# Kernel optimization log

Measured on AMD Instinct MI355X. Metric: run time of the kernel, lower is better.

Reference implementation:

```python
import jax, jax.numpy as jnp
import numpy as np


def setup_inputs() -> dict:
    key = jax.random.key(0)
    k1, k2 = jax.random.split(key)
    B, DIM, T, SIZE = 64, 512, 2048, 1024
    H = jax.random.normal(k1, (B, DIM, T), dtype=jnp.float32)
    units = jax.random.normal(k2, (DIM, SIZE), dtype=jnp.float32)
    return {"H": H, "units": units}


def reference(H, units):
    # H: (B, dim, T), units: (dim, size)
    # Original: C[b, s, t] = exp(-||H[b,:,t] - units[:,s]||^2) normalized over s.
    # exp(-d^2) / sum_s exp(-d^2) == softmax(-d^2, axis=s).
    Ht = jnp.swapaxes(H, 1, 2)                      # (B, T, dim)
    h_sq = jnp.sum(Ht * Ht, axis=-1, keepdims=True)  # (B, T, 1)
    m_sq = jnp.sum(units * units, axis=0)            # (size,)
    cross = jnp.einsum('btd,ds->bts', Ht, units)     # (B, T, size) GEMM
    sqdist = h_sq - 2.0 * cross + m_sq               # (B, T, size)
    C = jax.nn.softmax(-sqdist, axis=-1)             # normalize over codebook
    return jnp.swapaxes(C, 1, 2)                     # (B, size, T)
```

## Files before the change

### kernel.cpp

```cpp
#include <hip/hip_runtime.h>
#include <stdint.h>


typedef unsigned short u16;
typedef __attribute__((ext_vector_type(8))) short short8;
typedef __attribute__((ext_vector_type(4))) float f32x4;

#define B_DIM 64
#define DIM   512
#define T_DIM 2048
#define S_DIM 1024

#define SLOT   40960
#define A_LO   16384
#define B_HI   32768
#define B_LO   36864
#define MSQ_O  122880
#define REDM_O 126976
#define REDS_O 128000
#define SM_SZ  129024

__device__ __forceinline__ u16 f32_to_bf16(float f) {
  uint32_t u = __float_as_uint(f);
  uint32_t r = u + 0x7FFFu + ((u >> 16) & 1u);
  return (u16)(r >> 16);
}
__device__ __forceinline__ float bf16_to_f32(u16 h) {
  return __uint_as_float(((uint32_t)h) << 16);
}

__global__ __launch_bounds__(256) void k_prep_units(const float* __restrict__ units,
                                                    u16* __restrict__ Uh, u16* __restrict__ Ul,
                                                    float* __restrict__ msq) {
  const int s0 = blockIdx.x * 4;
  const int tid = threadIdx.x;
  const int lane = tid & 63, wv = tid >> 6;
  float acc0 = 0.f, acc1 = 0.f, acc2 = 0.f, acc3 = 0.f;
#pragma unroll
  for (int j = 0; j < 2; ++j) {
    const int d = tid + j * 256;
    const float4 v = *(const float4*)(units + (size_t)d * S_DIM + s0);
    acc0 += v.x * v.x; acc1 += v.y * v.y; acc2 += v.z * v.z; acc3 += v.w * v.w;
    u16 h;
    h = f32_to_bf16(v.x); Uh[(s0 + 0) * DIM + d] = h; Ul[(s0 + 0) * DIM + d] = f32_to_bf16(v.x - bf16_to_f32(h));
    h = f32_to_bf16(v.y); Uh[(s0 + 1) * DIM + d] = h; Ul[(s0 + 1) * DIM + d] = f32_to_bf16(v.y - bf16_to_f32(h));
    h = f32_to_bf16(v.z); Uh[(s0 + 2) * DIM + d] = h; Ul[(s0 + 2) * DIM + d] = f32_to_bf16(v.z - bf16_to_f32(h));
    h = f32_to_bf16(v.w); Uh[(s0 + 3) * DIM + d] = h; Ul[(s0 + 3) * DIM + d] = f32_to_bf16(v.w - bf16_to_f32(h));
  }
#pragma unroll
  for (int off = 1; off < 64; off <<= 1) {
    acc0 += __shfl_xor(acc0, off);
    acc1 += __shfl_xor(acc1, off);
    acc2 += __shfl_xor(acc2, off);
    acc3 += __shfl_xor(acc3, off);
  }
  __shared__ float part[4][4];
  if (lane == 0) { part[wv][0] = acc0; part[wv][1] = acc1; part[wv][2] = acc2; part[wv][3] = acc3; }
  __syncthreads();
  if (tid < 4) msq[s0 + tid] = part[0][tid] + part[1][tid] + part[2][tid] + part[3][tid];
}

__global__ __launch_bounds__(256) void k_prep_h(const float* __restrict__ H,
                                                u16* __restrict__ Hh, u16* __restrict__ Hl) {
  __shared__ float tile[64 * 68];
  const int t0 = blockIdx.x * 64, d0 = blockIdx.y * 64, b = blockIdx.z;
  const int tid = threadIdx.x;
#pragma unroll
  for (int j = 0; j < 4; ++j) {
    const int chunk = tid + j * 256;
    const int r = chunk >> 4, c4 = (chunk & 15) * 4;
    const float4 v = *(const float4*)(H + ((size_t)(b * DIM + d0 + r)) * T_DIM + t0 + c4);
    *(float4*)(&tile[r * 68 + c4]) = v;
  }
  __syncthreads();
#pragma unroll
  for (int j = 0; j < 2; ++j) {
    const int chunk = tid + j * 256;
    const int q = chunk >> 3, e8 = (chunk & 7) * 8;
    union { u16 us[8]; uint4 v4; } hi, lo;
#pragma unroll
    for (int k = 0; k < 8; ++k) {
      const float f = tile[(e8 + k) * 68 + q];
      const u16 h = f32_to_bf16(f);
      hi.us[k] = h;
      lo.us[k] = f32_to_bf16(f - bf16_to_f32(h));
    }
    const size_t o = ((size_t)(b * T_DIM + t0 + q)) * DIM + d0 + e8;
    *(uint4*)(Hh + o) = hi.v4;
    *(uint4*)(Hl + o) = lo.v4;
  }
}

__device__ __forceinline__ void gl16(const void* g, void* l) {
  __builtin_amdgcn_global_load_lds((const __attribute__((address_space(1))) void*)g,
                                   (__attribute__((address_space(3))) void*)l, 16, 0, 0);
}

#define WAITV(N) asm volatile("s_waitcnt vmcnt(" #N ")" ::: "memory")
#define SYNCPT() do { __builtin_amdgcn_s_barrier(); __builtin_amdgcn_sched_barrier(0); } while (0)
#define LGKM0()  do { asm volatile("s_waitcnt lgkmcnt(0)" ::: "memory"); __builtin_amdgcn_sched_barrier(0); } while (0)

__global__ __launch_bounds__(512, 2) void k_fused(const u16* __restrict__ Uh, const u16* __restrict__ Ul,
                                                  const u16* __restrict__ Hh, const u16* __restrict__ Hl,
                                                  const float* __restrict__ msq,
                                                  float* __restrict__ out) {
  __shared__ __align__(16) char sm[SM_SZ];
  const int tid = threadIdx.x;
  const int lane = tid & 63, wv = tid >> 6;
  const int sw = wv >> 1, tw = wv & 1;
  const int l15 = lane & 15, lhi = lane >> 4;

  const int t00 = blockIdx.x * 64;
  const int bb = blockIdx.y;

  const int rA0 = tid >> 2;
  const int csA = ((tid & 3) ^ (rA0 >> 1)) & 3;
  const size_t aBase0 = (size_t)rA0 * 1024 + (size_t)csA * 16;
  const size_t aBase1 = aBase0 + (size_t)128 * 1024;
  const int rB = (tid & 255) >> 2;
  const int csB = ((tid & 3) ^ (rB >> 1)) & 3;
  const size_t bBase = ((size_t)(bb * T_DIM + t00 + rB)) * 1024 + (size_t)csB * 16;
  const char* const pAh = (const char*)Uh;
  const char* const pAl = (const char*)Ul;
  const char* const pB  = (tid < 256) ? (const char*)Hh : (const char*)Hl;
  const int dT = tid * 16;

#define STAGE(SLOTBASE, J2) do {                                          \
    const size_t aoff = (size_t)((J2) >> 4) * 262144 + (size_t)((J2) & 15) * 64; \
    const size_t boff = (size_t)((J2) & 15) * 64;                         \
    char* d = (SLOTBASE);                                                 \
    gl16(pAh + aBase0 + aoff, d + dT);                                    \
    gl16(pAh + aBase1 + aoff, d + dT + 8192);                             \
    gl16(pAl + aBase0 + aoff, d + A_LO + dT);                             \
    gl16(pAl + aBase1 + aoff, d + A_LO + dT + 8192);                      \
    gl16(pB + bBase + boff, d + B_HI + dT);                               \
  } while (0)

  const int cidx = ((lhi) ^ (l15 >> 1)) & 3;
  const int offA = sw * 4096 + l15 * 64 + cidx * 16;
  const int offB = tw * 2048 + l15 * 64 + cidx * 16;

  f32x4 acc[4][4][2];
#pragma unroll
  for (int sc = 0; sc < 4; ++sc)
#pragma unroll
    for (int mt = 0; mt < 4; ++mt)
#pragma unroll
      for (int nt = 0; nt < 2; ++nt)
        acc[sc][mt][nt] = (f32x4){0.f, 0.f, 0.f, 0.f};

#define COMPUTE(SC) do {                                                  \
    const char* sl = sm + slotJ * SLOT;                                   \
    short8 ah[4], al[4], bh[2], bl[2];                                    \
    _Pragma("unroll") for (int mt = 0; mt < 4; ++mt) {                    \
      ah[mt] = *(const short8*)(sl + offA + mt * 1024);                   \
      al[mt] = *(const short8*)(sl + A_LO + offA + mt * 1024);            \
    }                                                                     \
    _Pragma("unroll") for (int nt = 0; nt < 2; ++nt) {                    \
      bh[nt] = *(const short8*)(sl + B_HI + offB + nt * 1024);            \
      bl[nt] = *(const short8*)(sl + B_LO + offB + nt * 1024);            \
    }                                                                     \
    LGKM0();                                                              \
    __builtin_amdgcn_s_setprio(1);                                        \
    _Pragma("unroll") for (int mt = 0; mt < 4; ++mt)                      \
      _Pragma("unroll") for (int nt = 0; nt < 2; ++nt) {                  \
        acc[SC][mt][nt] = __builtin_amdgcn_mfma_f32_16x16x32_bf16(ah[mt], bh[nt], acc[SC][mt][nt], 0, 0, 0); \
        acc[SC][mt][nt] = __builtin_amdgcn_mfma_f32_16x16x32_bf16(ah[mt], bl[nt], acc[SC][mt][nt], 0, 0, 0); \
        acc[SC][mt][nt] = __builtin_amdgcn_mfma_f32_16x16x32_bf16(al[mt], bh[nt], acc[SC][mt][nt], 0, 0, 0); \
      }                                                                   \
    __builtin_amdgcn_s_setprio(0);                                        \
  } while (0)

  if (tid < 256) gl16((const char*)msq + tid * 16, sm + MSQ_O + tid * 16);
  STAGE(sm + 0 * SLOT, 0);
  STAGE(sm + 1 * SLOT, 1);

  int slotJ = 0;
#pragma unroll
  for (int sc = 0; sc < 3; ++sc) {
#pragma unroll 1
    for (int k = 0; k < 16; ++k) {
      const int j = sc * 16 + k;
      int slot2 = slotJ + 2; if (slot2 >= 3) slot2 -= 3;
      STAGE(sm + slot2 * SLOT, j + 2);
      WAITV(10); SYNCPT();
      COMPUTE(sc);
      SYNCPT();
      slotJ = (slotJ == 2) ? 0 : slotJ + 1;
    }
  }
#pragma unroll 1
  for (int k = 0; k < 14; ++k) {
    const int j = 48 + k;
    int slot2 = slotJ + 2; if (slot2 >= 3) slot2 -= 3;
    STAGE(sm + slot2 * SLOT, j + 2);
    WAITV(10); SYNCPT();
    COMPUTE(3);
    SYNCPT();
    slotJ = (slotJ == 2) ? 0 : slotJ + 1;
  }
  WAITV(5); SYNCPT(); COMPUTE(3); SYNCPT();
  slotJ = (slotJ == 2) ? 0 : slotJ + 1;
  WAITV(0); SYNCPT(); COMPUTE(3); SYNCPT();

  const float* msql = (const float*)(sm + MSQ_O);
  float* redM = (float*)(sm + REDM_O);
  float* redS = (float*)(sm + REDS_O);

  float m0 = -3.0e38f, m1 = -3.0e38f;
#pragma unroll
  for (int sc = 0; sc < 4; ++sc)
#pragma unroll
    for (int mt = 0; mt < 4; ++mt) {
      const int sb = sc * 256 + sw * 64 + mt * 16 + lhi * 4;
      const f32x4 q = *(const f32x4*)(msql + sb);
#pragma unroll
      for (int r = 0; r < 4; ++r) {
        const float v0 = 2.f * acc[sc][mt][0][r] - q[r];
        const float v1 = 2.f * acc[sc][mt][1][r] - q[r];
        acc[sc][mt][0][r] = v0; acc[sc][mt][1][r] = v1;
        m0 = fmaxf(m0, v0); m1 = fmaxf(m1, v1);
      }
    }
  m0 = fmaxf(m0, __shfl_xor(m0, 16)); m0 = fmaxf(m0, __shfl_xor(m0, 32));
  m1 = fmaxf(m1, __shfl_xor(m1, 16)); m1 = fmaxf(m1, __shfl_xor(m1, 32));
  if (lane < 16) { redM[wv * 32 + lane] = m0; redM[wv * 32 + 16 + lane] = m1; }
  __syncthreads();
  float M0 = redM[tw * 32 + l15], M1 = redM[tw * 32 + 16 + l15];
#pragma unroll
  for (int w = 1; w < 4; ++w) {
    M0 = fmaxf(M0, redM[(tw + 2 * w) * 32 + l15]);
    M1 = fmaxf(M1, redM[(tw + 2 * w) * 32 + 16 + l15]);
  }
  float s0 = 0.f, s1 = 0.f;
#pragma unroll
  for (int sc = 0; sc < 4; ++sc)
#pragma unroll
    for (int mt = 0; mt < 4; ++mt)
#pragma unroll
      for (int r = 0; r < 4; ++r) {
        const float e0 = __expf(acc[sc][mt][0][r] - M0);
        const float e1 = __expf(acc[sc][mt][1][r] - M1);
        acc[sc][mt][0][r] = e0; acc[sc][mt][1][r] = e1;
        s0 += e0; s1 += e1;
      }
  s0 += __shfl_xor(s0, 16); s0 += __shfl_xor(s0, 32);
  s1 += __shfl_xor(s1, 16); s1 += __shfl_xor(s1, 32);
  if (lane < 16) { redS[wv * 32 + lane] = s0; redS[wv * 32 + 16 + lane] = s1; }
  __syncthreads();
  float S0 = redS[tw * 32 + l15], S1 = redS[tw * 32 + 16 + l15];
#pragma unroll
  for (int w = 1; w < 4; ++w) {
    S0 += redS[(tw + 2 * w) * 32 + l15];
    S1 += redS[(tw + 2 * w) * 32 + 16 + l15];
  }
  const float r0 = 1.0f / S0, r1 = 1.0f / S1;

  float* const outb = out + ((size_t)bb << 21);
  const int tbase = t00 + tw * 32 + l15;
#pragma unroll
  for (int sc = 0; sc < 4; ++sc)
#pragma unroll
    for (int mt = 0; mt < 4; ++mt) {
      const int sb = sc * 256 + sw * 64 + mt * 16 + lhi * 4;
#pragma unroll
      for (int r = 0; r < 4; ++r) {
        outb[(size_t)(sb + r) * T_DIM + tbase]      = acc[sc][mt][0][r] * r0;
        outb[(size_t)(sb + r) * T_DIM + tbase + 16] = acc[sc][mt][1][r] * r1;
      }
    }
}

extern "C" void kernel_launch(void* const* d_in, const int* in_sizes, int n_in,
                              void* d_out, int out_size, void* d_ws, size_t ws_size,
                              hipStream_t stream) {
  (void)in_sizes; (void)n_in; (void)out_size; (void)ws_size;
  const float* H = (const float*)d_in[0];
  const float* units = (const float*)d_in[1];
  float* out = (float*)d_out;
  char* ws = (char*)d_ws;
  u16* Hh = (u16*)(ws);
  u16* Hl = (u16*)(ws + 134217728);
  u16* Uh = (u16*)(ws + 268435456);
  u16* Ul = (u16*)(ws + 269484032);
  float* msq = (float*)(ws + 270532608);

  k_prep_units<<<dim3(S_DIM / 4), 256, 0, stream>>>(units, Uh, Ul, msq);
  k_prep_h<<<dim3(T_DIM / 64, DIM / 64, B_DIM), 256, 0, stream>>>(H, Hh, Hl);
  k_fused<<<dim3(T_DIM / 64, B_DIM), 512, 0, stream>>>(Uh, Ul, Hh, Hl, msq, out);
}
```

Measured before the change: 680.1 us.

## Switch fused GEMM-softmax to 32x32x16 MFMA with full-S tiles and double buffering

Replaces the 16x16x32 MFMA tiling, which walked four S-chunks across a 3-slot pipeline, with 32x32x16 MFMAs. Each of the 8 waves now owns 128 codebook rows over all 64 t-columns, with a 2-slot double buffer over K steps of 16 and a new LDS layout. The goal is fewer MFMA instructions and LDS reads per FLOP, plus a simpler reduction over 8 waves. In exchange it drops the LDS swizzle and the explicit lgkmcnt wait, so bank conflicts are possible, and LDS use grows, which may hurt the 2-blocks-per-CU occupancy target.

```diff
diff --git a/kernel.cpp b/kernel.cpp
--- a/kernel.cpp
+++ b/kernel.cpp
@@ -5,20 +5,20 @@
 typedef unsigned short u16;
 typedef __attribute__((ext_vector_type(8))) short short8;
 typedef __attribute__((ext_vector_type(4))) float f32x4;
+typedef __attribute__((ext_vector_type(16))) float f32x16;
 
 #define B_DIM 64
 #define DIM   512
 #define T_DIM 2048
 #define S_DIM 1024
 
-#define SLOT   40960
-#define A_LO   16384
-#define B_HI   32768
-#define B_LO   36864
-#define MSQ_O  122880
-#define REDM_O 126976
-#define REDS_O 128000
-#define SM_SZ  129024
+#define SLOT   69632
+#define A_LO   32768
+#define B_HI   65536
+#define MSQ_O  139264
+#define REDM_O 143360
+#define REDS_O 145408
+#define SM_SZ  147456
 
 __device__ __forceinline__ u16 f32_to_bf16(float f) {
   uint32_t u = __float_as_uint(f);
@@ -98,7 +98,6 @@
 
 #define WAITV(N) asm volatile("s_waitcnt vmcnt(" #N ")" ::: "memory")
 #define SYNCPT() do { __builtin_amdgcn_s_barrier(); __builtin_amdgcn_sched_barrier(0); } while (0)
-#define LGKM0()  do { asm volatile("s_waitcnt lgkmcnt(0)" ::: "memory"); __builtin_amdgcn_sched_barrier(0); } while (0)
 
 __global__ __launch_bounds__(512, 2) void k_fused(const u16* __restrict__ Uh, const u16* __restrict__ Ul,
                                                   const u16* __restrict__ Hh, const u16* __restrict__ Hl,
@@ -107,168 +106,158 @@
   __shared__ __align__(16) char sm[SM_SZ];
   const int tid = threadIdx.x;
   const int lane = tid & 63, wv = tid >> 6;
-  const int sw = wv >> 1, tw = wv & 1;
-  const int l15 = lane & 15, lhi = lane >> 4;
+  const int l31 = lane & 31, lhi = lane >> 5;
+  const int lane16 = lane * 16;
 
   const int t00 = blockIdx.x * 64;
   const int bb = blockIdx.y;
 
-  const int rA0 = tid >> 2;
-  const int csA = ((tid & 3) ^ (rA0 >> 1)) & 3;
-  const size_t aBase0 = (size_t)rA0 * 1024 + (size_t)csA * 16;
-  const size_t aBase1 = aBase0 + (size_t)128 * 1024;
-  const int rB = (tid & 255) >> 2;
-  const int csB = ((tid & 3) ^ (rB >> 1)) & 3;
-  const size_t bBase = ((size_t)(bb * T_DIM + t00 + rB)) * 1024 + (size_t)csB * 16;
+  int aSrc[4], aDst[4];
+#pragma unroll
+  for (int i = 0; i < 4; ++i) {
+    const int ci = tid + i * 512;
+    const int si = (ci >> 6) * 32 + (ci & 31);
+    aSrc[i] = si * 1024 + (((ci >> 5) & 1) << 4);
+    aDst[i] = ci * 16;
+  }
+  const int cB = tid & 127;
+  const int tB = (cB >> 6) * 32 + (cB & 31);
+  const size_t bSrc = ((size_t)(bb * T_DIM + t00 + tB)) * 1024 + (size_t)(((cB >> 5) & 1) << 4);
+  const int bDst = B_HI + tid * 16;
   const char* const pAh = (const char*)Uh;
   const char* const pAl = (const char*)Ul;
-  const char* const pB  = (tid < 256) ? (const char*)Hh : (const char*)Hl;
-  const int dT = tid * 16;
-
-#define STAGE(SLOTBASE, J2) do {                                          \
-    const size_t aoff = (size_t)((J2) >> 4) * 262144 + (size_t)((J2) & 15) * 64; \
-    const size_t boff = (size_t)((J2) & 15) * 64;                         \
-    char* d = (SLOTBASE);                                                 \
-    gl16(pAh + aBase0 + aoff, d + dT);                                    \
-    gl16(pAh + aBase1 + aoff, d + dT + 8192);                             \
-    gl16(pAl + aBase0 + aoff, d + A_LO + dT);                             \
-    gl16(pAl + aBase1 + aoff, d + A_LO + dT + 8192);                      \
-    gl16(pB + bBase + boff, d + B_HI + dT);                               \
+  const char* const pBsel = (tid < 128) ? (const char*)Hh : (const char*)Hl;
+
+#define STAGE(SLOTB, KS) do {                                             \
+    const int ko = (KS) * 32;                                             \
+    char* d = sm + (SLOTB);                                               \
+    gl16(pAh + aSrc[0] + ko, d + aDst[0]);                                \
+    gl16(pAh + aSrc[1] + ko, d + aDst[1]);                                \
+    gl16(pAh + aSrc[2] + ko, d + aDst[2]);                                \
+    gl16(pAh + aSrc[3] + ko, d + aDst[3]);                                \
+    gl16(pAl + aSrc[0] + ko, d + A_LO + aDst[0]);                         \
+    gl16(pAl + aSrc[1] + ko, d + A_LO + aDst[1]);                         \
+    gl16(pAl + aSrc[2] + ko, d + A_LO + aDst[2]);                         \
+    gl16(pAl + aSrc[3] + ko, d + A_LO + aDst[3]);                         \
+    if (tid < 256) gl16(pBsel + bSrc + ko, d + bDst);                     \
   } while (0)
 
-  const int cidx = ((lhi) ^ (l15 >> 1)) & 3;
-  const int offA = sw * 4096 + l15 * 64 + cidx * 16;
-  const int offB = tw * 2048 + l15 * 64 + cidx * 16;
-
-  f32x4 acc[4][4][2];
-#pragma unroll
-  for (int sc = 0; sc < 4; ++sc)
-#pragma unroll
-    for (int mt = 0; mt < 4; ++mt)
-#pragma unroll
-      for (int nt = 0; nt < 2; ++nt)
-        acc[sc][mt][nt] = (f32x4){0.f, 0.f, 0.f, 0.f};
-
-#define COMPUTE(SC) do {                                                  \
-    const char* sl = sm + slotJ * SLOT;                                   \
+  const int sw = wv;
+
+  f32x16 acc[4][2];
+#pragma unroll
+  for (int mt = 0; mt < 4; ++mt)
+#pragma unroll
+    for (int nt = 0; nt < 2; ++nt)
+#pragma unroll
+      for (int r = 0; r < 16; ++r)
+        acc[mt][nt][r] = 0.f;
+
+#define COMPUTE(SLOTB) do {                                               \
+    const char* sl = sm + (SLOTB);                                        \
     short8 ah[4], al[4], bh[2], bl[2];                                    \
     _Pragma("unroll") for (int mt = 0; mt < 4; ++mt) {                    \
-      ah[mt] = *(const short8*)(sl + offA + mt * 1024);                   \
-      al[mt] = *(const short8*)(sl + A_LO + offA + mt * 1024);            \
+      ah[mt] = *(const short8*)(sl + (sw * 4 + mt) * 1024 + lane16);      \
+      al[mt] = *(const short8*)(sl + A_LO + (sw * 4 + mt) * 1024 + lane16); \
     }                                                                     \
     _Pragma("unroll") for (int nt = 0; nt < 2; ++nt) {                    \
-      bh[nt] = *(const short8*)(sl + B_HI + offB + nt * 1024);            \
-      bl[nt] = *(const short8*)(sl + B_LO + offB + nt * 1024);            \
+      bh[nt] = *(const short8*)(sl + B_HI + nt * 1024 + lane16);          \
+      bl[nt] = *(const short8*)(sl + B_HI + 2048 + nt * 1024 + lane16);   \
     }                                                                     \
-    LGKM0();                                                              \
     __builtin_amdgcn_s_setprio(1);                                        \
     _Pragma("unroll") for (int mt = 0; mt < 4; ++mt)                      \
       _Pragma("unroll") for (int nt = 0; nt < 2; ++nt) {                  \
-        acc[SC][mt][nt] = __builtin_amdgcn_mfma_f32_16x16x32_bf16(ah[mt], bh[nt], acc[SC][mt][nt], 0, 0, 0); \
-        acc[SC][mt][nt] = __builtin_amdgcn_mfma_f32_16x16x32_bf16(ah[mt], bl[nt], acc[SC][mt][nt], 0, 0, 0); \
-        acc[SC][mt][nt] = __builtin_amdgcn_mfma_f32_16x16x32_bf16(al[mt], bh[nt], acc[SC][mt][nt], 0, 0, 0); \
+        acc[mt][nt] = __builtin_amdgcn_mfma_f32_32x32x16_bf16(ah[mt], bh[nt], acc[mt][nt], 0, 0, 0); \
+        acc[mt][nt] = __builtin_amdgcn_mfma_f32_32x32x16_bf16(ah[mt], bl[nt], acc[mt][nt], 0, 0, 0); \
+        acc[mt][nt] = __builtin_amdgcn_mfma_f32_32x32x16_bf16(al[mt], bh[nt], acc[mt][nt], 0, 0, 0); \
       }                                                                   \
     __builtin_amdgcn_s_setprio(0);                                        \
   } while (0)
 
   if (tid < 256) gl16((const char*)msq + tid * 16, sm + MSQ_O + tid * 16);
-  STAGE(sm + 0 * SLOT, 0);
-  STAGE(sm + 1 * SLOT, 1);
-
-  int slotJ = 0;
-#pragma unroll
-  for (int sc = 0; sc < 3; ++sc) {
+  STAGE(0, 0);
+  STAGE(SLOT, 1);
+
 #pragma unroll 1
-    for (int k = 0; k < 16; ++k) {
-      const int j = sc * 16 + k;
-      int slot2 = slotJ + 2; if (slot2 >= 3) slot2 -= 3;
-      STAGE(sm + slot2 * SLOT, j + 2);
-      WAITV(10); SYNCPT();
-      COMPUTE(sc);
-      SYNCPT();
-      slotJ = (slotJ == 2) ? 0 : slotJ + 1;
-    }
-  }
-#pragma unroll 1
-  for (int k = 0; k < 14; ++k) {
-    const int j = 48 + k;
-    int slot2 = slotJ + 2; if (slot2 >= 3) slot2 -= 3;
-    STAGE(sm + slot2 * SLOT, j + 2);
-    WAITV(10); SYNCPT();
-    COMPUTE(3);
+  for (int k = 0; k < 31; ++k) {
+    WAITV(8);
     SYNCPT();
-    slotJ = (slotJ == 2) ? 0 : slotJ + 1;
-  }
-  WAITV(5); SYNCPT(); COMPUTE(3); SYNCPT();
-  slotJ = (slotJ == 2) ? 0 : slotJ + 1;
-  WAITV(0); SYNCPT(); COMPUTE(3); SYNCPT();
+    COMPUTE((k & 1) * SLOT);
+    SYNCPT();
+    if (k < 30) STAGE((k & 1) * SLOT, k + 2);
+  }
+  WAITV(0);
+  SYNCPT();
+  COMPUTE(SLOT);
 
   const float* msql = (const float*)(sm + MSQ_O);
   float* redM = (float*)(sm + REDM_O);
   float* redS = (float*)(sm + REDS_O);
 
-  float m0 = -3.0e38f, m1 = -3.0e38f;
-#pragma unroll
-  for (int sc = 0; sc < 4; ++sc)
-#pragma unroll
-    for (int mt = 0; mt < 4; ++mt) {
-      const int sb = sc * 256 + sw * 64 + mt * 16 + lhi * 4;
-      const f32x4 q = *(const f32x4*)(msql + sb);
+  float mx0 = -3.0e38f, mx1 = -3.0e38f;
+#pragma unroll
+  for (int mt = 0; mt < 4; ++mt) {
+    const int sb = sw * 128 + mt * 32 + lhi * 4;
+#pragma unroll
+    for (int q = 0; q < 4; ++q) {
+      const f32x4 mq = *(const f32x4*)(msql + sb + q * 8);
 #pragma unroll
       for (int r = 0; r < 4; ++r) {
-        const float v0 = 2.f * acc[sc][mt][0][r] - q[r];
-        const float v1 = 2.f * acc[sc][mt][1][r] - q[r];
-        acc[sc][mt][0][r] = v0; acc[sc][mt][1][r] = v1;
-        m0 = fmaxf(m0, v0); m1 = fmaxf(m1, v1);
+        const int reg = q * 4 + r;
+        const float v0 = 2.f * acc[mt][0][reg] - mq[r];
+        const float v1 = 2.f * acc[mt][1][reg] - mq[r];
+        acc[mt][0][reg] = v0; acc[mt][1][reg] = v1;
+        mx0 = fmaxf(mx0, v0); mx1 = fmaxf(mx1, v1);
       }
     }
-  m0 = fmaxf(m0, __shfl_xor(m0, 16)); m0 = fmaxf(m0, __shfl_xor(m0, 32));
-  m1 = fmaxf(m1, __shfl_xor(m1, 16)); m1 = fmaxf(m1, __shfl_xor(m1, 32));
-  if (lane < 16) { redM[wv * 32 + lane] = m0; redM[wv * 32 + 16 + lane] = m1; }
-  __syncthreads();
-  float M0 = redM[tw * 32 + l15], M1 = redM[tw * 32 + 16 + l15];
-#pragma unroll
-  for (int w = 1; w < 4; ++w) {
-    M0 = fmaxf(M0, redM[(tw + 2 * w) * 32 + l15]);
-    M1 = fmaxf(M1, redM[(tw + 2 * w) * 32 + 16 + l15]);
+  }
+  mx0 = fmaxf(mx0, __shfl_xor(mx0, 32));
+  mx1 = fmaxf(mx1, __shfl_xor(mx1, 32));
+  if (lane < 32) { redM[wv * 64 + l31] = mx0; redM[wv * 64 + 32 + l31] = mx1; }
+  __syncthreads();
+  float M0 = redM[l31], M1 = redM[32 + l31];
+#pragma unroll
+  for (int w = 1; w < 8; ++w) {
+    M0 = fmaxf(M0, redM[w * 64 + l31]);
+    M1 = fmaxf(M1, redM[w * 64 + 32 + l31]);
   }
   float s0 = 0.f, s1 = 0.f;
 #pragma unroll
-  for (int sc = 0; sc < 4; ++sc)
-#pragma unroll
-    for (int mt = 0; mt < 4; ++mt)
+  for (int mt = 0; mt < 4; ++mt)
+#pragma unroll
+    for (int reg = 0; reg < 16; ++reg) {
+      const float e0 = __expf(acc[mt][0][reg] - M0);
+      const float e1 = __expf(acc[mt][1][reg] - M1);
+      acc[mt][0][reg] = e0; acc[mt][1][reg] = e1;
+      s0 += e0; s1 += e1;
+    }
+  s0 += __shfl_xor(s0, 32);
+  s1 += __shfl_xor(s1, 32);
+  if (lane < 32) { redS[wv * 64 + l31] = s0; redS[wv * 64 + 32 + l31] = s1; }
+  __syncthreads();
+  float S0 = redS[l31], S1 = redS[32 + l31];
+#pragma unroll
+  for (int w = 1; w < 8; ++w) {
+    S0 += redS[w * 64 + l31];
+    S1 += redS[w * 64 + 32 + l31];
+  }
+  const float r0 = 1.0f / S0, r1 = 1.0f / S1;
+
+  float* const outb = out + ((size_t)bb << 21);
+  const int tc0 = t00 + l31, tc1 = t00 + 32 + l31;
+#pragma unroll
+  for (int mt = 0; mt < 4; ++mt) {
+    const int sb = sw * 128 + mt * 32 + lhi * 4;
+#pragma unroll
+    for (int q = 0; q < 4; ++q)
 #pragma unroll
       for (int r = 0; r < 4; ++r) {
-        const float e0 = __expf(acc[sc][mt][0][r] - M0);
-        const float e1 = __expf(acc[sc][mt][1][r] - M1);
-        acc[sc][mt][0][r] = e0; acc[sc][mt][1][r] = e1;
-        s0 += e0; s1 += e1;
+        const int srow = sb + q * 8 + r;
+        const int reg = q * 4 + r;
+        outb[(size_t)srow * T_DIM + tc0] = acc[mt][0][reg] * r0;
+        outb[(size_t)srow * T_DIM + tc1] = acc[mt][1][reg] * r1;
       }
-  s0 += __shfl_xor(s0, 16); s0 += __shfl_xor(s0, 32);
-  s1 += __shfl_xor(s1, 16); s1 += __shfl_xor(s1, 32);
-  if (lane < 16) { redS[wv * 32 + lane] = s0; redS[wv * 32 + 16 + lane] = s1; }
-  __syncthreads();
-  float S0 = redS[tw * 32 + l15], S1 = redS[tw * 32 + 16 + l15];
-#pragma unroll
-  for (int w = 1; w < 4; ++w) {
-    S0 += redS[(tw + 2 * w) * 32 + l15];
-    S1 += redS[(tw + 2 * w) * 32 + 16 + l15];
-  }
-  const float r0 = 1.0f / S0, r1 = 1.0f / S1;
-
-  float* const outb = out + ((size_t)bb << 21);
-  const int tbase = t00 + tw * 32 + l15;
-#pragma unroll
-  for (int sc = 0; sc < 4; ++sc)
-#pragma unroll
-    for (int mt = 0; mt < 4; ++mt) {
-      const int sb = sc * 256 + sw * 64 + mt * 16 + lhi * 4;
-#pragma unroll
-      for (int r = 0; r < 4; ++r) {
-        outb[(size_t)(sb + r) * T_DIM + tbase]      = acc[sc][mt][0][r] * r0;
-        outb[(size_t)(sb + r) * T_DIM + tbase + 16] = acc[sc][mt][1][r] * r1;
-      }
-    }
+  }
 }
 
 extern "C" void kernel_launch(void* const* d_in, const int* in_sizes, int n_in,
```

After: 840.2 us. 23.6% more time.
